# Kernel tuning notes

Hardware: AMD Instinct MI355X
Metric: run time of the kernel (lower is better)

The kernel has to match this reference:

```python
import jax, jax.numpy as jnp
import numpy as np

NUM_HEADS = 8
CHUNK = 64          # dialtion / chunck_size
EPS = 1e-5          # InstanceNorm1d eps
NEG = -1e9


def setup_inputs() -> dict:
    key = jax.random.key(0)
    ks = jax.random.split(key, 8)
    N, C, T = 4, 512, 4096
    x = jax.random.normal(ks[0], (N, C, T), dtype=jnp.float32)
    q = jax.random.normal(ks[1], (N, C, T), dtype=jnp.float32)
    k = jax.random.normal(ks[2], (N, C, T), dtype=jnp.float32)
    v = jax.random.normal(ks[3], (N, C, T), dtype=jnp.float32)
    masks = jnp.ones((N, 1, T), dtype=jnp.float32)
    s = 1.0 / np.sqrt(C)
    W_in = jax.random.normal(ks[4], (3 * C, C), dtype=jnp.float32) * s   # packed q/k/v in-proj
    b_in = jnp.zeros((3 * C,), dtype=jnp.float32)
    W_out = jax.random.normal(ks[5], (C, C), dtype=jnp.float32) * s     # out-proj
    b_out = jnp.zeros((C,), dtype=jnp.float32)
    return {"x": x, "q": q, "k": k, "v": v, "masks": masks,
            "W_in": W_in, "b_in": b_in, "W_out": W_out, "b_out": b_out}


def _chunk_attn(q, k, v, masks, W_in, b_in, W_out, b_out):
    # q,k,v: [N, C, T]; masks: [N, 1, T]
    N, C, T = q.shape
    H, Dh = NUM_HEADS, C // NUM_HEADS
    nc = T // CHUNK
    Wq, Wk, Wv = jnp.split(W_in, 3, axis=0)
    bq, bk, bv = jnp.split(b_in, 3, axis=0)

    def proj(t, W, b):
        # [N,C,T] -> chunked heads [N, nc, CHUNK, H, Dh]
        t = t.transpose(0, 2, 1) @ W.T + b            # [N, T, C]
        return t.reshape(N, nc, CHUNK, H, Dh)

    qh = proj(q, Wq, bq)
    kh = proj(k, Wk, bk)
    vh = proj(v, Wv, bv)

    scale = 1.0 / jnp.sqrt(jnp.asarray(Dh, q.dtype))
    # intra-chunk scores: [N, nc, H, CHUNK, CHUNK]
    scores = jnp.einsum('bnqhd,bnkhd->bnhqk', qh, kh) * scale
    km = masks[:, 0, :].reshape(N, nc, CHUNK)         # key validity per chunk
    scores = scores + jnp.where(km[:, :, None, None, :] > 0, 0.0, NEG)
    attn = jax.nn.softmax(scores, axis=-1)
    out = jnp.einsum('bnhqk,bnkhd->bnqhd', attn, vh).reshape(N, T, C)
    out = out @ W_out.T + b_out                        # [N, T, C]
    out = out.transpose(0, 2, 1) * masks               # [N, C, T], re-mask
    return out


def reference(x, q, k, v, masks, W_in, b_in, W_out, b_out):
    out = _chunk_attn(q, k, v, masks, W_in, b_in, W_out, b_out) + x
    # InstanceNorm1d (affine=False): normalize each (n, c) row over T
    mu = jnp.mean(out, axis=2, keepdims=True)
    var = jnp.mean(jnp.square(out - mu), axis=2, keepdims=True)
    return (out - mu) * jax.lax.rsqrt(var + EPS)
```

## Files before the change

kernel.cpp:

```cpp
#include <hip/hip_runtime.h>
#include <hip/hip_bf16.h>

#define NB 4
#define CC 512
#define TT 4096
#define HH 8
#define DHH 64
#define C3 1536
#define NTC (NB*TT*CC)

typedef __attribute__((ext_vector_type(4))) float f32x4;
typedef __attribute__((ext_vector_type(8))) short short8;
typedef unsigned short ushort;

__device__ __forceinline__ ushort f2bf(float f){
    union { float f; unsigned u; } x; x.f = f;
    unsigned r = x.u + 0x7fffu + ((x.u >> 16) & 1u);
    return (ushort)(r >> 16);
}

__global__ __launch_bounds__(256) void cvt_w(const float* __restrict__ Wi,
                                             const float* __restrict__ Wo,
                                             ushort* __restrict__ Wb,
                                             ushort* __restrict__ Wob){
    int t = blockIdx.x * 256 + threadIdx.x;
    const float* src; ushort* dst; int idx;
    if (t < 196608){ src = Wi; dst = Wb;  idx = t; }
    else           { src = Wo; dst = Wob; idx = t - 196608; }
    f32x4 v = *((const f32x4*)src + idx);
    ushort4 o;
    o.x = f2bf(v[0]); o.y = f2bf(v[1]); o.z = f2bf(v[2]); o.w = f2bf(v[3]);
    *((ushort4*)dst + idx) = o;
}

__global__ __launch_bounds__(256) void transpose_cvt(const float* __restrict__ q,
                                                     const float* __restrict__ k,
                                                     const float* __restrict__ v,
                                                     ushort* __restrict__ XT){
    __shared__ float sT[64][65];
    int b = blockIdx.x;
    int tch = b % 64;  b /= 64;
    int cch = b % 8;   b /= 8;
    int n   = b % 4;   b /= 4;
    int which = b;
    const float* src = (which == 0) ? q : (which == 1) ? k : v;
    const float* base = src + (size_t)n*CC*TT + (size_t)(cch*64)*TT + (size_t)tch*64;
    for (int i = 0; i < 4; ++i){
        int f = i*256 + threadIdx.x;
        int t4 = f & 15, c = f >> 4;
        f32x4 val = *(const f32x4*)(base + (size_t)c*TT + t4*4);
        for (int j = 0; j < 4; ++j) sT[t4*4 + j][c] = val[j];
    }
    __syncthreads();
    ushort* dst = XT + (size_t)which*NTC + ((size_t)n*TT + (size_t)tch*64)*CC + cch*64;
    for (int i = 0; i < 4; ++i){
        int f = i*256 + threadIdx.x;
        int c4 = f & 15, t = f >> 4;
        ushort4 o;
        o.x = f2bf(sT[t][c4*4+0]); o.y = f2bf(sT[t][c4*4+1]);
        o.z = f2bf(sT[t][c4*4+2]); o.w = f2bf(sT[t][c4*4+3]);
        *(ushort4*)(dst + (size_t)t*CC + c4*4) = o;
    }
}

__global__ __launch_bounds__(256) void proj_gemm(const ushort* __restrict__ XT,
                                                 const ushort* __restrict__ Wb,
                                                 const float* __restrict__ b_in,
                                                 ushort* __restrict__ P){
    __shared__ ushort sA[128][72];
    __shared__ ushort sB[128][72];
    const int tid = threadIdx.x;
    const int co0 = blockIdx.x * 128;
    const int m0  = blockIdx.y * 128;
    const int which = co0 >> 9;
    const ushort* Abase = XT + (size_t)which*NTC + (size_t)m0*CC;
    const ushort* Bbase = Wb + (size_t)co0*CC;
    const int w = tid >> 6, lane = tid & 63;
    const int wr = w >> 1, wc = w & 1;
    const int l15 = lane & 15, quad = lane >> 4;
    f32x4 acc[4][4] = {};
    for (int kb = 0; kb < 8; ++kb){
        __syncthreads();
        for (int i = 0; i < 4; ++i){
            int f = i*256 + tid;
            int r = f >> 3, c8 = f & 7;
            *(int4*)&sA[r][c8*8] = *(const int4*)(Abase + (size_t)r*CC + kb*64 + c8*8);
            *(int4*)&sB[r][c8*8] = *(const int4*)(Bbase + (size_t)r*CC + kb*64 + c8*8);
        }
        __syncthreads();
        for (int ks = 0; ks < 2; ++ks){
            short8 aF[4], bF[4];
            for (int mi = 0; mi < 4; ++mi)
                aF[mi] = *(const short8*)&sA[wr*64 + mi*16 + l15][ks*32 + quad*8];
            for (int ni = 0; ni < 4; ++ni)
                bF[ni] = *(const short8*)&sB[wc*64 + ni*16 + l15][ks*32 + quad*8];
            for (int mi = 0; mi < 4; ++mi)
                for (int ni = 0; ni < 4; ++ni)
                    acc[mi][ni] = __builtin_amdgcn_mfma_f32_16x16x32_bf16(
                        aF[mi], bF[ni], acc[mi][ni], 0, 0, 0);
        }
    }
    float bj[4];
    for (int ni = 0; ni < 4; ++ni) bj[ni] = b_in[co0 + wc*64 + ni*16 + l15];
    for (int mi = 0; mi < 4; ++mi){
        int m = m0 + wr*64 + mi*16 + quad*4;
        for (int ni = 0; ni < 4; ++ni){
            int co = co0 + wc*64 + ni*16 + l15;
            ushort* dst = P + (size_t)m*C3 + co;
            for (int r = 0; r < 4; ++r)
                dst[(size_t)r*C3] = f2bf(acc[mi][ni][r] + bj[ni]);
        }
    }
}

__global__ __launch_bounds__(256) void attn_kernel(const ushort* __restrict__ P,
                                                   const float* __restrict__ masks,
                                                   ushort* __restrict__ ctx){
    __shared__ ushort sQ[64][72], sK[64][72], sVt[64][72], sP[64][72];
    int bid = blockIdx.x;
    int h = bid & 7, ch = (bid >> 3) & 63, n = bid >> 9;
    const int tid = threadIdx.x, lane = tid & 63, w = tid >> 6;
    const int l15 = lane & 15, quad = lane >> 4;
    const size_t rowbase = (size_t)n*TT + (size_t)ch*64;
    for (int i = 0; i < 2; ++i){
        int f = i*256 + tid;
        int r = f >> 3, c8 = f & 7;
        const ushort* src = P + (rowbase + r)*C3 + h*64 + c8*8;
        *(int4*)&sQ[r][c8*8] = *(const int4*)(src);
        *(int4*)&sK[r][c8*8] = *(const int4*)(src + 512);
        int4 vv = *(const int4*)(src + 1024);
        const ushort* pv = (const ushort*)&vv;
        for (int j = 0; j < 8; ++j) sVt[c8*8 + j][r] = pv[j];
    }
    __syncthreads();
    const int m0w = w*16;
    short8 aQ[2]; f32x4 accS[4] = {};
    for (int ks = 0; ks < 2; ++ks)
        aQ[ks] = *(const short8*)&sQ[m0w + l15][ks*32 + quad*8];
    for (int ni = 0; ni < 4; ++ni)
        for (int ks = 0; ks < 2; ++ks){
            short8 bK = *(const short8*)&sK[ni*16 + l15][ks*32 + quad*8];
            accS[ni] = __builtin_amdgcn_mfma_f32_16x16x32_bf16(aQ[ks], bK, accS[ni], 0,0,0);
        }
    float madd[4];
    for (int ni = 0; ni < 4; ++ni){
        float mv = masks[(size_t)n*TT + ch*64 + ni*16 + l15];
        madd[ni] = (mv > 0.f) ? 0.f : -1e9f;
    }
    float s[4][4];
    for (int ni = 0; ni < 4; ++ni)
        for (int r = 0; r < 4; ++r) s[ni][r] = accS[ni][r]*0.125f + madd[ni];
    float ex[4][4];
    for (int r = 0; r < 4; ++r){
        float m1 = fmaxf(fmaxf(s[0][r], s[1][r]), fmaxf(s[2][r], s[3][r]));
        for (int d = 1; d < 16; d <<= 1) m1 = fmaxf(m1, __shfl_xor(m1, d));
        float a = 0.f;
        for (int ni = 0; ni < 4; ++ni){ float e = __expf(s[ni][r] - m1); ex[ni][r] = e; a += e; }
        for (int d = 1; d < 16; d <<= 1) a += __shfl_xor(a, d);
        float rs = 1.0f / a;
        for (int ni = 0; ni < 4; ++ni)
            sP[m0w + quad*4 + r][ni*16 + l15] = f2bf(ex[ni][r] * rs);
    }
    short8 aP[2]; f32x4 accO[4] = {};
    for (int ks = 0; ks < 2; ++ks)
        aP[ks] = *(const short8*)&sP[m0w + l15][ks*32 + quad*8];
    for (int ni = 0; ni < 4; ++ni)
        for (int ks = 0; ks < 2; ++ks){
            short8 bV = *(const short8*)&sVt[ni*16 + l15][ks*32 + quad*8];
            accO[ni] = __builtin_amdgcn_mfma_f32_16x16x32_bf16(aP[ks], bV, accO[ni], 0,0,0);
        }
    for (int ni = 0; ni < 4; ++ni)
        for (int r = 0; r < 4; ++r){
            size_t row = rowbase + m0w + quad*4 + r;
            ctx[row*CC + h*64 + ni*16 + l15] = f2bf(accO[ni][r]);
        }
}

__global__ __launch_bounds__(256) void out_gemm(const ushort* __restrict__ ctx,
                                                const ushort* __restrict__ Wob,
                                                const float* __restrict__ b_out,
                                                const float* __restrict__ x,
                                                const float* __restrict__ masks,
                                                float* __restrict__ out){
    __shared__ ushort sA[128][72];
    __shared__ ushort sB[128][72];
    const int tid = threadIdx.x;
    const int co0 = blockIdx.x * 128;
    const int m0  = blockIdx.y * 128;
    const int n = m0 >> 12, t0 = m0 & 4095;
    const ushort* Abase = ctx + (size_t)m0*CC;
    const ushort* Bbase = Wob + (size_t)co0*CC;
    const int w = tid >> 6, lane = tid & 63;
    const int wr = w >> 1, wc = w & 1;
    const int l15 = lane & 15, quad = lane >> 4;
    f32x4 acc[4][4] = {};
    for (int kb = 0; kb < 8; ++kb){
        __syncthreads();
        for (int i = 0; i < 4; ++i){
            int f = i*256 + tid;
            int r = f >> 3, c8 = f & 7;
            *(int4*)&sA[r][c8*8] = *(const int4*)(Abase + (size_t)r*CC + kb*64 + c8*8);
            *(int4*)&sB[r][c8*8] = *(const int4*)(Bbase + (size_t)r*CC + kb*64 + c8*8);
        }
        __syncthreads();
        for (int ks = 0; ks < 2; ++ks){
            short8 aF[4], bF[4];
            for (int mi = 0; mi < 4; ++mi)
                aF[mi] = *(const short8*)&sA[wr*64 + mi*16 + l15][ks*32 + quad*8];
            for (int ni = 0; ni < 4; ++ni)
                bF[ni] = *(const short8*)&sB[wc*64 + ni*16 + l15][ks*32 + quad*8];
            for (int mi = 0; mi < 4; ++mi)
                for (int ni = 0; ni < 4; ++ni)
                    acc[mi][ni] = __builtin_amdgcn_mfma_f32_16x16x32_bf16(
                        aF[mi], bF[ni], acc[mi][ni], 0, 0, 0);
        }
    }
    float bo[4];
    for (int ni = 0; ni < 4; ++ni) bo[ni] = b_out[co0 + wc*64 + ni*16 + l15];
    for (int mi = 0; mi < 4; ++mi){
        int t = t0 + wr*64 + mi*16 + quad*4;
        f32x4 mk = *(const f32x4*)(masks + (size_t)n*TT + t);
        for (int ni = 0; ni < 4; ++ni){
            int co = co0 + wc*64 + ni*16 + l15;
            const f32x4 xv = *(const f32x4*)(x + ((size_t)n*CC + co)*TT + t);
            f32x4 o;
            for (int r = 0; r < 4; ++r)
                o[r] = (acc[mi][ni][r] + bo[ni]) * mk[r] + xv[r];
            *(f32x4*)(out + ((size_t)n*CC + co)*TT + t) = o;
        }
    }
}

__global__ __launch_bounds__(256) void inorm(float* __restrict__ out){
    __shared__ float sS[4], sQ2[4];
    float* row = out + (size_t)blockIdx.x * TT;
    f32x4 vbuf[4];
    float s = 0.f, ss = 0.f;
    for (int i = 0; i < 4; ++i){
        f32x4 vv = *(const f32x4*)(row + (size_t)(i*256 + threadIdx.x)*4);
        vbuf[i] = vv;
        for (int r = 0; r < 4; ++r){ s += vv[r]; ss += vv[r]*vv[r]; }
    }
    for (int d = 1; d < 64; d <<= 1){ s += __shfl_xor(s, d); ss += __shfl_xor(ss, d); }
    int w = threadIdx.x >> 6;
    if ((threadIdx.x & 63) == 0){ sS[w] = s; sQ2[w] = ss; }
    __syncthreads();
    s  = sS[0] + sS[1] + sS[2] + sS[3];
    ss = sQ2[0] + sQ2[1] + sQ2[2] + sQ2[3];
    float mean = s * (1.0f/TT);
    float var  = ss * (1.0f/TT) - mean*mean;
    float rstd = rsqrtf(var + 1e-5f);
    for (int i = 0; i < 4; ++i){
        f32x4 vv = vbuf[i], o;
        for (int r = 0; r < 4; ++r) o[r] = (vv[r] - mean) * rstd;
        *(f32x4*)(row + (size_t)(i*256 + threadIdx.x)*4) = o;
    }
}

extern "C" void kernel_launch(void* const* d_in, const int* in_sizes, int n_in,
                              void* d_out, int out_size, void* d_ws, size_t ws_size,
                              hipStream_t stream) {
    const float* x     = (const float*)d_in[0];
    const float* q     = (const float*)d_in[1];
    const float* k     = (const float*)d_in[2];
    const float* v     = (const float*)d_in[3];
    const float* masks = (const float*)d_in[4];
    const float* W_in  = (const float*)d_in[5];
    const float* b_in  = (const float*)d_in[6];
    const float* W_out = (const float*)d_in[7];
    const float* b_out = (const float*)d_in[8];
    float* out = (float*)d_out;

    ushort* ws  = (ushort*)d_ws;
    ushort* XT  = ws;
    ushort* Wb  = ws + (size_t)3*NTC;
    ushort* Wob = Wb + 786432;
    ushort* P   = Wob + 262144;
    ushort* ctx = ws;

    cvt_w<<<1024, 256, 0, stream>>>(W_in, W_out, Wb, Wob);
    transpose_cvt<<<6144, 256, 0, stream>>>(q, k, v, XT);
    proj_gemm<<<dim3(12, 128), 256, 0, stream>>>(XT, Wb, b_in, P);
    attn_kernel<<<2048, 256, 0, stream>>>(P, masks, ctx);
    out_gemm<<<dim3(4, 128), 256, 0, stream>>>(ctx, Wob, b_out, x, masks, out);
    inorm<<<2048, 256, 0, stream>>>(out);
}
```

Measured before the change: 268.1 us.

## Use direct global-to-LDS loads with XOR swizzle and pre-transposed V layout

Replaces register-staged shared-memory tile loads in both GEMMs and the attention kernel with global_load_lds direct copies into an XOR-swizzled LDS layout, removing padding and bank conflicts. The projection GEMM now writes V directly in a per-head transposed layout so the attention kernel no longer does a scalar transpose into shared memory. Block indices are remapped to a 1D grid with M-tile interleaving for better L2 reuse of weight/activation tiles. This adds layout complexity and relies on the async LDS load path; the V transposed store uses strided 8-byte writes.

```diff
diff --git a/kernel.cpp b/kernel.cpp
--- a/kernel.cpp
+++ b/kernel.cpp
@@ -4,9 +4,8 @@
 #define NB 4
 #define CC 512
 #define TT 4096
-#define HH 8
-#define DHH 64
 #define C3 1536
+#define CQK 1024
 #define NTC (NB*TT*CC)
 
 typedef __attribute__((ext_vector_type(4))) float f32x4;
@@ -17,6 +16,12 @@
     union { float f; unsigned u; } x; x.f = f;
     unsigned r = x.u + 0x7fffu + ((x.u >> 16) & 1u);
     return (ushort)(r >> 16);
+}
+
+__device__ __forceinline__ void gload16(const void* g, void* l){
+    __builtin_amdgcn_global_load_lds((const __attribute__((address_space(1))) void*)g,
+                                     (__attribute__((address_space(3))) void*)l,
+                                     16, 0, 0);
 }
 
 __global__ __launch_bounds__(256) void cvt_w(const float* __restrict__ Wi,
@@ -66,80 +71,121 @@
 __global__ __launch_bounds__(256) void proj_gemm(const ushort* __restrict__ XT,
                                                  const ushort* __restrict__ Wb,
                                                  const float* __restrict__ b_in,
-                                                 ushort* __restrict__ P){
-    __shared__ ushort sA[128][72];
-    __shared__ ushort sB[128][72];
+                                                 ushort* __restrict__ P,
+                                                 ushort* __restrict__ Vt){
+    __shared__ ushort sA[128*64];
+    __shared__ ushort sB[128*64];
     const int tid = threadIdx.x;
-    const int co0 = blockIdx.x * 128;
-    const int m0  = blockIdx.y * 128;
+    const int bid = blockIdx.x;
+    const int mtile  = ((bid & 7) << 4) | ((bid >> 3) & 15);
+    const int cotile = bid >> 7;
+    const int co0 = cotile * 128;
+    const int m0  = mtile * 128;
     const int which = co0 >> 9;
     const ushort* Abase = XT + (size_t)which*NTC + (size_t)m0*CC;
     const ushort* Bbase = Wb + (size_t)co0*CC;
     const int w = tid >> 6, lane = tid & 63;
     const int wr = w >> 1, wc = w & 1;
     const int l15 = lane & 15, quad = lane >> 4;
+
+    const ushort* gA[4]; const ushort* gB[4];
+    ushort* lA[4]; ushort* lB[4];
+    for (int i = 0; i < 4; ++i){
+        int slot = i*256 + tid;
+        int m = slot >> 3, k8 = slot & 7, kk = k8 ^ (m & 7);
+        gA[i] = Abase + (size_t)m*CC + kk*8;
+        gB[i] = Bbase + (size_t)m*CC + kk*8;
+        int lbase = (i*256 + (tid & ~63)) * 8;
+        lA[i] = sA + lbase;  lB[i] = sB + lbase;
+    }
+
     f32x4 acc[4][4] = {};
     for (int kb = 0; kb < 8; ++kb){
         __syncthreads();
         for (int i = 0; i < 4; ++i){
-            int f = i*256 + tid;
-            int r = f >> 3, c8 = f & 7;
-            *(int4*)&sA[r][c8*8] = *(const int4*)(Abase + (size_t)r*CC + kb*64 + c8*8);
-            *(int4*)&sB[r][c8*8] = *(const int4*)(Bbase + (size_t)r*CC + kb*64 + c8*8);
+            gload16(gA[i] + kb*64, lA[i]);
+            gload16(gB[i] + kb*64, lB[i]);
         }
         __syncthreads();
         for (int ks = 0; ks < 2; ++ks){
             short8 aF[4], bF[4];
-            for (int mi = 0; mi < 4; ++mi)
-                aF[mi] = *(const short8*)&sA[wr*64 + mi*16 + l15][ks*32 + quad*8];
-            for (int ni = 0; ni < 4; ++ni)
-                bF[ni] = *(const short8*)&sB[wc*64 + ni*16 + l15][ks*32 + quad*8];
+            for (int mi = 0; mi < 4; ++mi){
+                int m = wr*64 + mi*16 + l15;
+                aF[mi] = *(const short8*)&sA[(m*8 + ((ks*4 + quad) ^ (m & 7)))*8];
+            }
+            for (int ni = 0; ni < 4; ++ni){
+                int m = wc*64 + ni*16 + l15;
+                bF[ni] = *(const short8*)&sB[(m*8 + ((ks*4 + quad) ^ (m & 7)))*8];
+            }
             for (int mi = 0; mi < 4; ++mi)
                 for (int ni = 0; ni < 4; ++ni)
                     acc[mi][ni] = __builtin_amdgcn_mfma_f32_16x16x32_bf16(
                         aF[mi], bF[ni], acc[mi][ni], 0, 0, 0);
         }
     }
+
     float bj[4];
     for (int ni = 0; ni < 4; ++ni) bj[ni] = b_in[co0 + wc*64 + ni*16 + l15];
-    for (int mi = 0; mi < 4; ++mi){
-        int m = m0 + wr*64 + mi*16 + quad*4;
-        for (int ni = 0; ni < 4; ++ni){
-            int co = co0 + wc*64 + ni*16 + l15;
-            ushort* dst = P + (size_t)m*C3 + co;
-            for (int r = 0; r < 4; ++r)
-                dst[(size_t)r*C3] = f2bf(acc[mi][ni][r] + bj[ni]);
+    if (which < 2){
+        for (int mi = 0; mi < 4; ++mi){
+            int m = m0 + wr*64 + mi*16 + quad*4;
+            for (int ni = 0; ni < 4; ++ni){
+                int col = (co0 & 511) + wc*64 + ni*16 + l15;
+                ushort* dst = P + (size_t)m*CQK + which*512 + col;
+                for (int r = 0; r < 4; ++r)
+                    dst[(size_t)r*CQK] = f2bf(acc[mi][ni][r] + bj[ni]);
+            }
+        }
+    } else {
+        for (int mi = 0; mi < 4; ++mi){
+            int m = m0 + wr*64 + mi*16 + quad*4;
+            int n = m >> 12, t = m & 4095;
+            for (int ni = 0; ni < 4; ++ni){
+                int col = (co0 & 511) + wc*64 + ni*16 + l15;
+                int h = col >> 6, d = col & 63;
+                ushort4 o4;
+                o4.x = f2bf(acc[mi][ni][0] + bj[ni]);
+                o4.y = f2bf(acc[mi][ni][1] + bj[ni]);
+                o4.z = f2bf(acc[mi][ni][2] + bj[ni]);
+                o4.w = f2bf(acc[mi][ni][3] + bj[ni]);
+                *(ushort4*)&Vt[(((size_t)n*8 + h)*64 + d)*TT + t] = o4;
+            }
         }
     }
 }
 
 __global__ __launch_bounds__(256) void attn_kernel(const ushort* __restrict__ P,
+                                                   const ushort* __restrict__ Vt,
                                                    const float* __restrict__ masks,
                                                    ushort* __restrict__ ctx){
-    __shared__ ushort sQ[64][72], sK[64][72], sVt[64][72], sP[64][72];
+    __shared__ ushort sQ[64*64], sK[64*64], sV[64*64];
+    __shared__ ushort sP[64][72];
     int bid = blockIdx.x;
     int h = bid & 7, ch = (bid >> 3) & 63, n = bid >> 9;
     const int tid = threadIdx.x, lane = tid & 63, w = tid >> 6;
     const int l15 = lane & 15, quad = lane >> 4;
     const size_t rowbase = (size_t)n*TT + (size_t)ch*64;
     for (int i = 0; i < 2; ++i){
-        int f = i*256 + tid;
-        int r = f >> 3, c8 = f & 7;
-        const ushort* src = P + (rowbase + r)*C3 + h*64 + c8*8;
-        *(int4*)&sQ[r][c8*8] = *(const int4*)(src);
-        *(int4*)&sK[r][c8*8] = *(const int4*)(src + 512);
-        int4 vv = *(const int4*)(src + 1024);
-        const ushort* pv = (const ushort*)&vv;
-        for (int j = 0; j < 8; ++j) sVt[c8*8 + j][r] = pv[j];
+        int slot = i*256 + tid;
+        int r = slot >> 3, k8 = slot & 7, kk = k8 ^ (r & 7);
+        int lbase = (i*256 + (tid & ~63)) * 8;
+        const ushort* gq = P + (rowbase + r)*CQK + h*64 + kk*8;
+        gload16(gq,        sQ + lbase);
+        gload16(gq + 512,  sK + lbase);
+        const ushort* gv = Vt + (((size_t)n*8 + h)*64 + r)*TT + ch*64 + kk*8;
+        gload16(gv,        sV + lbase);
     }
     __syncthreads();
     const int m0w = w*16;
     short8 aQ[2]; f32x4 accS[4] = {};
-    for (int ks = 0; ks < 2; ++ks)
-        aQ[ks] = *(const short8*)&sQ[m0w + l15][ks*32 + quad*8];
+    for (int ks = 0; ks < 2; ++ks){
+        int m = m0w + l15;
+        aQ[ks] = *(const short8*)&sQ[(m*8 + ((ks*4 + quad) ^ (m & 7)))*8];
+    }
     for (int ni = 0; ni < 4; ++ni)
         for (int ks = 0; ks < 2; ++ks){
-            short8 bK = *(const short8*)&sK[ni*16 + l15][ks*32 + quad*8];
+            int m = ni*16 + l15;
+            short8 bK = *(const short8*)&sK[(m*8 + ((ks*4 + quad) ^ (m & 7)))*8];
             accS[ni] = __builtin_amdgcn_mfma_f32_16x16x32_bf16(aQ[ks], bK, accS[ni], 0,0,0);
         }
     float madd[4];
@@ -166,7 +212,8 @@
         aP[ks] = *(const short8*)&sP[m0w + l15][ks*32 + quad*8];
     for (int ni = 0; ni < 4; ++ni)
         for (int ks = 0; ks < 2; ++ks){
-            short8 bV = *(const short8*)&sVt[ni*16 + l15][ks*32 + quad*8];
+            int m = ni*16 + l15;
+            short8 bV = *(const short8*)&sV[(m*8 + ((ks*4 + quad) ^ (m & 7)))*8];
             accO[ni] = __builtin_amdgcn_mfma_f32_16x16x32_bf16(aP[ks], bV, accO[ni], 0,0,0);
         }
     for (int ni = 0; ni < 4; ++ni)
@@ -182,33 +229,50 @@
                                                 const float* __restrict__ x,
                                                 const float* __restrict__ masks,
                                                 float* __restrict__ out){
-    __shared__ ushort sA[128][72];
-    __shared__ ushort sB[128][72];
+    __shared__ ushort sA[128*64];
+    __shared__ ushort sB[128*64];
     const int tid = threadIdx.x;
-    const int co0 = blockIdx.x * 128;
-    const int m0  = blockIdx.y * 128;
+    const int bid = blockIdx.x;
+    const int mtile  = ((bid & 7) << 4) | ((bid >> 3) & 15);
+    const int cotile = bid >> 7;
+    const int co0 = cotile * 128;
+    const int m0  = mtile * 128;
     const int n = m0 >> 12, t0 = m0 & 4095;
     const ushort* Abase = ctx + (size_t)m0*CC;
     const ushort* Bbase = Wob + (size_t)co0*CC;
     const int w = tid >> 6, lane = tid & 63;
     const int wr = w >> 1, wc = w & 1;
     const int l15 = lane & 15, quad = lane >> 4;
+
+    const ushort* gA[4]; const ushort* gB[4];
+    ushort* lA[4]; ushort* lB[4];
+    for (int i = 0; i < 4; ++i){
+        int slot = i*256 + tid;
+        int m = slot >> 3, k8 = slot & 7, kk = k8 ^ (m & 7);
+        gA[i] = Abase + (size_t)m*CC + kk*8;
+        gB[i] = Bbase + (size_t)m*CC + kk*8;
+        int lbase = (i*256 + (tid & ~63)) * 8;
+        lA[i] = sA + lbase;  lB[i] = sB + lbase;
+    }
+
     f32x4 acc[4][4] = {};
     for (int kb = 0; kb < 8; ++kb){
         __syncthreads();
         for (int i = 0; i < 4; ++i){
-            int f = i*256 + tid;
-            int r = f >> 3, c8 = f & 7;
-            *(int4*)&sA[r][c8*8] = *(const int4*)(Abase + (size_t)r*CC + kb*64 + c8*8);
-            *(int4*)&sB[r][c8*8] = *(const int4*)(Bbase + (size_t)r*CC + kb*64 + c8*8);
+            gload16(gA[i] + kb*64, lA[i]);
+            gload16(gB[i] + kb*64, lB[i]);
         }
         __syncthreads();
         for (int ks = 0; ks < 2; ++ks){
             short8 aF[4], bF[4];
-            for (int mi = 0; mi < 4; ++mi)
-                aF[mi] = *(const short8*)&sA[wr*64 + mi*16 + l15][ks*32 + quad*8];
-            for (int ni = 0; ni < 4; ++ni)
-                bF[ni] = *(const short8*)&sB[wc*64 + ni*16 + l15][ks*32 + quad*8];
+            for (int mi = 0; mi < 4; ++mi){
+                int m = wr*64 + mi*16 + l15;
+                aF[mi] = *(const short8*)&sA[(m*8 + ((ks*4 + quad) ^ (m & 7)))*8];
+            }
+            for (int ni = 0; ni < 4; ++ni){
+                int m = wc*64 + ni*16 + l15;
+                bF[ni] = *(const short8*)&sB[(m*8 + ((ks*4 + quad) ^ (m & 7)))*8];
+            }
             for (int mi = 0; mi < 4; ++mi)
                 for (int ni = 0; ni < 4; ++ni)
                     acc[mi][ni] = __builtin_amdgcn_mfma_f32_16x16x32_bf16(
@@ -276,12 +340,13 @@
     ushort* Wb  = ws + (size_t)3*NTC;
     ushort* Wob = Wb + 786432;
     ushort* P   = Wob + 262144;
+    ushort* Vt  = P + (size_t)NB*TT*CQK;
     ushort* ctx = ws;
 
     cvt_w<<<1024, 256, 0, stream>>>(W_in, W_out, Wb, Wob);
     transpose_cvt<<<6144, 256, 0, stream>>>(q, k, v, XT);
-    proj_gemm<<<dim3(12, 128), 256, 0, stream>>>(XT, Wb, b_in, P);
-    attn_kernel<<<2048, 256, 0, stream>>>(P, masks, ctx);
-    out_gemm<<<dim3(4, 128), 256, 0, stream>>>(ctx, Wob, b_out, x, masks, out);
+    proj_gemm<<<1536, 256, 0, stream>>>(XT, Wb, b_in, P, Vt);
+    attn_kernel<<<2048, 256, 0, stream>>>(P, Vt, masks, ctx);
+    out_gemm<<<512, 256, 0, stream>>>(ctx, Wob, b_out, x, masks, out);
     inorm<<<2048, 256, 0, stream>>>(out);
 }
```

Result: no change. 269.1 us (+0.4%).
